# Kernel tuning notes

Measured on AMD Instinct MI355X. Metric: run time of the kernel, lower is better.

## Reference

```python
import jax, jax.numpy as jnp
import numpy as np

NEG = -1e30  # finite stand-in for log(0); safe for logaddexp and its gradient


def setup_inputs() -> dict:
    key = jax.random.key(0)
    k1, k2 = jax.random.split(key)
    B, T, C, U = 256, 512, 128, 128
    logits = jax.random.normal(k1, (B, T, C), dtype=jnp.float32)
    y_pred = jax.nn.softmax(logits, axis=-1)  # ctc_batch_cost expects probabilities
    y_true = jax.random.randint(k2, (B, U), 0, C - 1)  # labels exclude blank=C-1
    return {"y_true": y_true, "y_pred": y_pred}


def _ctc_batch_cost(y_true, y_pred):
    """Keras-style CTC: blank = num_classes-1, logp = log(y_pred + 1e-7),
    full input_length = T and label_length = U for every row (as in the layer).
    Returns loss of shape [B, 1]."""
    B, T, C = y_pred.shape
    U = y_true.shape[1]
    blank = C - 1
    S = 2 * U + 1  # extended label: blank-interleaved
    logp = jnp.log(y_pred + 1e-7)  # [B,T,C], keras epsilon

    # extended label sequence z = [blank, l1, blank, l2, ..., lU, blank]
    ext = jnp.full((B, S), blank, dtype=y_true.dtype).at[:, 1::2].set(y_true)

    # lp[t,b,s] = logp[b,t,ext[b,s]]
    lp = jnp.take_along_axis(logp, jnp.broadcast_to(ext[:, None, :], (B, T, S)), axis=2)
    lp = jnp.transpose(lp, (1, 0, 2))  # [T,B,S]

    # skip transition s-2 -> s allowed iff z[s] != blank and z[s] != z[s-2]
    ext_m2 = jnp.pad(ext, ((0, 0), (2, 0)), constant_values=blank)[:, :S]
    skip = (ext != blank) & (ext != ext_m2)
    skip = skip.at[:, :2].set(False)  # no s-2 predecessor for s in {0,1}

    alpha0 = jnp.full((B, S), NEG, dtype=logp.dtype)
    alpha0 = alpha0.at[:, 0].set(lp[0, :, 0]).at[:, 1].set(lp[0, :, 1])

    def step(a, lp_t):
        a1 = jnp.pad(a, ((0, 0), (1, 0)), constant_values=NEG)[:, :S]
        a2 = jnp.pad(a, ((0, 0), (2, 0)), constant_values=NEG)[:, :S]
        a2 = jnp.where(skip, a2, NEG)
        a = jnp.logaddexp(jnp.logaddexp(a, a1), a2) + lp_t
        return a, None

    aT, _ = jax.lax.scan(step, alpha0, lp[1:])
    loss = -jnp.logaddexp(aT[:, S - 1], aT[:, S - 2])
    return loss[:, None]  # [B,1], matching ctc_batch_cost output shape


def reference(y_true, y_pred):
    # The layer returns y_pred and registers the loss via add_loss; the loss is
    # the actual computation of interest, so we return it.
    return _ctc_batch_cost(y_true, y_pred)
```

## Files before the change

kernel.cpp:

```cpp
#include <hip/hip_runtime.h>

#define EPSF 1e-7f

typedef unsigned int u32;
typedef _Float16 h2_t __attribute__((ext_vector_type(2)));

#define DPPF0(x, ctrl) \
    __int_as_float(__builtin_amdgcn_update_dpp(0, __float_as_int(x), ctrl, 0xF, 0xF, false))

__device__ __forceinline__ float f_rcp(float x) { return __builtin_amdgcn_rcpf(x); }
__device__ __forceinline__ float wave_shr1_f(float x) { return DPPF0(x, 0x138); }

__device__ __forceinline__ float wave_max64(float x) {
    x = fmaxf(x, DPPF0(x, 0x111));
    x = fmaxf(x, DPPF0(x, 0x112));
    x = fmaxf(x, DPPF0(x, 0x114));
    x = fmaxf(x, DPPF0(x, 0x118));
    x = fmaxf(x, DPPF0(x, 0x142));
    x = fmaxf(x, DPPF0(x, 0x143));
    return __int_as_float(__builtin_amdgcn_readlane(__float_as_int(x), 63));
}

__device__ __forceinline__ float wave_sum64(float x) {
    x += DPPF0(x, 0x111);
    x += DPPF0(x, 0x112);
    x += DPPF0(x, 0x114);
    x += DPPF0(x, 0x118);
    x += DPPF0(x, 0x142);
    x += DPPF0(x, 0x143);
    return __int_as_float(__builtin_amdgcn_readlane(__float_as_int(x), 63));
}

#define STEPQ(PW_, PBE_) do { \
    const h2_t h_ = __builtin_bit_cast(h2_t, PW_); \
    const float rpb_ = f_rcp(PBE_); \
    const float q1 = ((float)h_.x + EPSF) * rpb_; \
    const float q3 = ((float)h_.y + EPSF) * rpb_; \
    const float n3 = wave_shr1_f(u3); \
    const float t1 = fmaf(m1, n3, u0 + u1); \
    const float t3 = fmaf(m3, u1, u2 + u3); \
    u4 = u4 + u3; \
    u3 = t3 * q3; \
    u2 = u2 + u1; \
    u1 = t1 * q1; \
    u0 = u0 + n3; \
} while (0)

#define SNAP2(RM, LM) do { \
    float mm_ = fmaxf(fmaxf(u0, u1), fmaxf(u2, fmaxf(u3, u4))); \
    mm_ = wave_max64(mm_); \
    RM = f_rcp(mm_); \
    LM = __logf(mm_); \
} while (0)

#define APPLY2(RM, LM) do { \
    u0 *= RM; u1 *= RM; u2 *= RM; u3 *= RM; u4 *= RM; \
    O += LM; \
} while (0)

#define LDW(X, BASE) do { \
    X##k0 = pkl[(BASE) + 0][lane]; X##k1 = pkl[(BASE) + 1][lane]; \
    X##k2 = pkl[(BASE) + 2][lane]; X##k3 = pkl[(BASE) + 3][lane]; \
    X##k4 = pkl[(BASE) + 4][lane]; X##k5 = pkl[(BASE) + 5][lane]; \
    X##k6 = pkl[(BASE) + 6][lane]; X##k7 = pkl[(BASE) + 7][lane]; \
    X##b0 = pbl[(BASE) + 0]; X##b1 = pbl[(BASE) + 1]; \
    X##b2 = pbl[(BASE) + 2]; X##b3 = pbl[(BASE) + 3]; \
    X##b4 = pbl[(BASE) + 4]; X##b5 = pbl[(BASE) + 5]; \
    X##b6 = pbl[(BASE) + 6]; X##b7 = pbl[(BASE) + 7]; \
} while (0)

#define CONS8W(X) do { \
    STEPQ(X##k0, X##b0 + EPSF); STEPQ(X##k1, X##b1 + EPSF); APPLY2(rmA, lmA); \
    STEPQ(X##k2, X##b2 + EPSF); STEPQ(X##k3, X##b3 + EPSF); SNAP2(rmB, lmB); \
    STEPQ(X##k4, X##b4 + EPSF); STEPQ(X##k5, X##b5 + EPSF); APPLY2(rmB, lmB); \
    STEPQ(X##k6, X##b6 + EPSF); STEPQ(X##k7, X##b7 + EPSF); SNAP2(rmA, lmA); \
} while (0)

#define CONS0W(X) do { \
    STEPQ(X##k1, X##b1 + EPSF); STEPQ(X##k2, X##b2 + EPSF); APPLY2(rmA, lmA); \
    STEPQ(X##k3, X##b3 + EPSF); STEPQ(X##k4, X##b4 + EPSF); SNAP2(rmB, lmB); \
    STEPQ(X##k5, X##b5 + EPSF); STEPQ(X##k6, X##b6 + EPSF); APPLY2(rmB, lmB); \
    STEPQ(X##k7, X##b7 + EPSF); SNAP2(rmA, lmA); \
} while (0)

__global__ __launch_bounds__(256, 1) void ctc_fused512(
        const int* __restrict__ y_true, const float* __restrict__ y_pred,
        float* __restrict__ out) {
    __shared__ u32   pkl[512][64];
    __shared__ float pbl[512];

    const int b    = blockIdx.x;
    const int tid  = threadIdx.x;
    const int w    = tid >> 6;
    const int lane = tid & 63;
    const float* __restrict__ yp = y_pred + (size_t)b * (512 * 128);

    const int2 lc = ((const int2*)(y_true + (size_t)b * 128))[lane];
    const int c1 = lc.x, c3 = lc.y;

    {
        const int t0 = w * 128;
        const float* __restrict__ rp = yp + (size_t)t0 * 128;
#pragma unroll 8
        for (int r = 0; r < 128; ++r) {
            const float p1 = rp[r * 128 + c1];
            const float p3 = rp[r * 128 + c3];
            const u32 wd = (u32)__builtin_bit_cast(unsigned short, (_Float16)p1)
                         | ((u32)__builtin_bit_cast(unsigned short, (_Float16)p3) << 16);
            pkl[t0 + r][lane] = wd;
        }
        pbl[t0 + lane]      = rp[(size_t)lane * 128 + 127];
        pbl[t0 + 64 + lane] = rp[(size_t)(64 + lane) * 128 + 127];
    }
    __syncthreads();
    if (w != 0) return;

    const int cp = __builtin_amdgcn_update_dpp(0, c3, 0x138, 0xF, 0xF, false);
    const float m1 = (lane > 0 && c1 != cp) ? 1.f : 0.f;
    const float m3 = (c3 != c1) ? 1.f : 0.f;

    float bls = 0.f;
#pragma unroll
    for (int k = 0; k < 8; ++k) {
        const int t = lane * 8 + k;
        if (t >= 1) bls += __logf(pbl[t] + EPSF);
    }
    bls = wave_sum64(bls);

    float u0, u1, u2 = 0.f, u3 = 0.f, u4 = 0.f;
    u0 = (lane == 0) ? yp[127] + EPSF : 0.f;
    u1 = (lane == 0) ? yp[c1] + EPSF : 0.f;
    float O = 0.f;
    float rmA = 1.0f, lmA = 0.0f, rmB = 1.0f, lmB = 0.0f;

    u32 Ak0, Ak1, Ak2, Ak3, Ak4, Ak5, Ak6, Ak7;
    u32 Bk0, Bk1, Bk2, Bk3, Bk4, Bk5, Bk6, Bk7;
    float Ab0, Ab1, Ab2, Ab3, Ab4, Ab5, Ab6, Ab7;
    float Bb0, Bb1, Bb2, Bb3, Bb4, Bb5, Bb6, Bb7;

    LDW(A, 0);
    LDW(B, 8);
    CONS0W(A);

    for (int j = 0; j < 31; ++j) {
        LDW(A, 16 * j + 16); CONS8W(B);
        LDW(B, 16 * j + 24); CONS8W(A);
    }
    CONS8W(B);

    if (lane == 63) out[b] = -(O + bls + __logf(u3 + u4));
}

__global__ __launch_bounds__(64, 1) void ctc_scan_generic(
        const int* __restrict__ y_true, const float* __restrict__ y_pred,
        float* __restrict__ out, int T, int C, int U) {
    const int b    = blockIdx.x;
    const int lane = threadIdx.x;
    const int blank = C - 1;
    const float* __restrict__ yp = y_pred + (size_t)b * T * C;

    const int2 lc = ((const int2*)(y_true + (size_t)b * U))[lane];
    const int c1 = lc.x, c3 = lc.y;
    const int cp = __builtin_amdgcn_update_dpp(0, c3, 0x138, 0xF, 0xF, false);
    const float m1 = (lane > 0 && c1 != cp) ? 1.f : 0.f;
    const float m3 = (c3 != c1) ? 1.f : 0.f;

    float u0, u1, u2 = 0.f, u3 = 0.f, u4 = 0.f;
    u0 = (lane == 0) ? yp[blank] + EPSF : 0.f;
    u1 = (lane == 0) ? yp[c1] + EPSF : 0.f;
    float O = 0.f;
    float rmA = 1.0f, lmA = 0.0f;
    int kren = 0;

    for (int t = 1; t < T; ++t) {
        const float* row = yp + (size_t)t * C;
        const float pbe = row[blank] + EPSF;
        const float rpb = f_rcp(pbe);
        const float q1  = (row[c1] + EPSF) * rpb;
        const float q3  = (row[c3] + EPSF) * rpb;
        const float n3  = wave_shr1_f(u3);
        const float t1  = fmaf(m1, n3, u0 + u1);
        const float t3  = fmaf(m3, u1, u2 + u3);
        u4 = u4 + u3;
        u3 = t3 * q3;
        u2 = u2 + u1;
        u1 = t1 * q1;
        u0 = u0 + n3;
        O += __logf(pbe);
        if (++kren == 4) { SNAP2(rmA, lmA); APPLY2(rmA, lmA); kren = 0; }
    }
    if (lane == 63) out[b] = -(O + __logf(u3 + u4));
}

extern "C" void kernel_launch(void* const* d_in, const int* in_sizes, int n_in,
                              void* d_out, int out_size, void* d_ws, size_t ws_size,
                              hipStream_t stream) {
    const int*   y_true = (const int*)d_in[0];
    const float* y_pred = (const float*)d_in[1];
    float*       out    = (float*)d_out;

    const int B = out_size;
    const int U = in_sizes[0] / B;
    const int C = 128;
    const int T = in_sizes[1] / (B * C);

    if (T == 512 && C == 128 && U == 128) {
        ctc_fused512<<<B, 256, 0, stream>>>(y_true, y_pred, out);
    } else {
        ctc_scan_generic<<<B, 64, 0, stream>>>(y_true, y_pred, out, T, C, U);
    }
}
```

Measured before the change: 51.48 us.

## Stage y_pred rows through LDS with coalesced loads and precompute bf16 ratios

Replaces the per-lane gather of label probabilities from global memory with coalesced float4 loads of 32-row tiles into a shared staging buffer, double-buffered through registers. All four waves now compute the blank-normalised ratios q1,q3 during the prologue and pack them as bf16 pairs, so the serial scan wave no longer needs a reciprocal and extra per-step multiply. The aim is to cut uncoalesced global traffic and shorten the serial critical path. It adds 32 barriers and more shared memory, and bf16 ratios carry less mantissa precision than the previous fp16 probabilities.

```diff
diff --git a/kernel.cpp b/kernel.cpp
--- a/kernel.cpp
+++ b/kernel.cpp
@@ -3,7 +3,6 @@
 #define EPSF 1e-7f
 
 typedef unsigned int u32;
-typedef _Float16 h2_t __attribute__((ext_vector_type(2)));
 
 #define DPPF0(x, ctrl) \
     __int_as_float(__builtin_amdgcn_update_dpp(0, __float_as_int(x), ctrl, 0xF, 0xF, false))
@@ -31,11 +30,17 @@
     return __int_as_float(__builtin_amdgcn_readlane(__float_as_int(x), 63));
 }
 
-#define STEPQ(PW_, PBE_) do { \
-    const h2_t h_ = __builtin_bit_cast(h2_t, PW_); \
-    const float rpb_ = f_rcp(PBE_); \
-    const float q1 = ((float)h_.x + EPSF) * rpb_; \
-    const float q3 = ((float)h_.y + EPSF) * rpb_; \
+__device__ __forceinline__ u32 pack_bf2(float a, float b) {
+    u32 ua = __float_as_uint(a), ub = __float_as_uint(b);
+    ua += 0x7FFFu + ((ua >> 16) & 1u);
+    ub += 0x7FFFu + ((ub >> 16) & 1u);
+    return (ua >> 16) | (ub & 0xFFFF0000u);
+}
+
+#define STEPQ(PW_) do { \
+    const u32 w_ = (PW_); \
+    const float q1 = __uint_as_float(w_ << 16); \
+    const float q3 = __uint_as_float(w_ & 0xFFFF0000u); \
     const float n3 = wave_shr1_f(u3); \
     const float t1 = fmaf(m1, n3, u0 + u1); \
     const float t3 = fmaf(m3, u1, u2 + u3); \
@@ -59,35 +64,32 @@
 } while (0)
 
 #define LDW(X, BASE) do { \
-    X##k0 = pkl[(BASE) + 0][lane]; X##k1 = pkl[(BASE) + 1][lane]; \
-    X##k2 = pkl[(BASE) + 2][lane]; X##k3 = pkl[(BASE) + 3][lane]; \
-    X##k4 = pkl[(BASE) + 4][lane]; X##k5 = pkl[(BASE) + 5][lane]; \
-    X##k6 = pkl[(BASE) + 6][lane]; X##k7 = pkl[(BASE) + 7][lane]; \
-    X##b0 = pbl[(BASE) + 0]; X##b1 = pbl[(BASE) + 1]; \
-    X##b2 = pbl[(BASE) + 2]; X##b3 = pbl[(BASE) + 3]; \
-    X##b4 = pbl[(BASE) + 4]; X##b5 = pbl[(BASE) + 5]; \
-    X##b6 = pbl[(BASE) + 6]; X##b7 = pbl[(BASE) + 7]; \
+    X##0 = qkl[(BASE) + 0][lane]; X##1 = qkl[(BASE) + 1][lane]; \
+    X##2 = qkl[(BASE) + 2][lane]; X##3 = qkl[(BASE) + 3][lane]; \
+    X##4 = qkl[(BASE) + 4][lane]; X##5 = qkl[(BASE) + 5][lane]; \
+    X##6 = qkl[(BASE) + 6][lane]; X##7 = qkl[(BASE) + 7][lane]; \
 } while (0)
 
 #define CONS8W(X) do { \
-    STEPQ(X##k0, X##b0 + EPSF); STEPQ(X##k1, X##b1 + EPSF); APPLY2(rmA, lmA); \
-    STEPQ(X##k2, X##b2 + EPSF); STEPQ(X##k3, X##b3 + EPSF); SNAP2(rmB, lmB); \
-    STEPQ(X##k4, X##b4 + EPSF); STEPQ(X##k5, X##b5 + EPSF); APPLY2(rmB, lmB); \
-    STEPQ(X##k6, X##b6 + EPSF); STEPQ(X##k7, X##b7 + EPSF); SNAP2(rmA, lmA); \
+    STEPQ(X##0); STEPQ(X##1); APPLY2(rmA, lmA); \
+    STEPQ(X##2); STEPQ(X##3); SNAP2(rmB, lmB); \
+    STEPQ(X##4); STEPQ(X##5); APPLY2(rmB, lmB); \
+    STEPQ(X##6); STEPQ(X##7); SNAP2(rmA, lmA); \
 } while (0)
 
 #define CONS0W(X) do { \
-    STEPQ(X##k1, X##b1 + EPSF); STEPQ(X##k2, X##b2 + EPSF); APPLY2(rmA, lmA); \
-    STEPQ(X##k3, X##b3 + EPSF); STEPQ(X##k4, X##b4 + EPSF); SNAP2(rmB, lmB); \
-    STEPQ(X##k5, X##b5 + EPSF); STEPQ(X##k6, X##b6 + EPSF); APPLY2(rmB, lmB); \
-    STEPQ(X##k7, X##b7 + EPSF); SNAP2(rmA, lmA); \
-} while (0)
-
-__global__ __launch_bounds__(256, 1) void ctc_fused512(
+    STEPQ(X##1); STEPQ(X##2); APPLY2(rmA, lmA); \
+    STEPQ(X##3); STEPQ(X##4); SNAP2(rmB, lmB); \
+    STEPQ(X##5); STEPQ(X##6); APPLY2(rmB, lmB); \
+    STEPQ(X##7); SNAP2(rmA, lmA); \
+} while (0)
+
+__global__ __launch_bounds__(256, 1) void ctc_fused512b(
         const int* __restrict__ y_true, const float* __restrict__ y_pred,
         float* __restrict__ out) {
-    __shared__ u32   pkl[512][64];
+    __shared__ u32   qkl[512][64];
     __shared__ float pbl[512];
+    __shared__ float stage[32][128];
 
     const int b    = blockIdx.x;
     const int tid  = threadIdx.x;
@@ -98,21 +100,57 @@
     const int2 lc = ((const int2*)(y_true + (size_t)b * 128))[lane];
     const int c1 = lc.x, c3 = lc.y;
 
+    float4 rg[4];
     {
-        const int t0 = w * 128;
-        const float* __restrict__ rp = yp + (size_t)t0 * 128;
-#pragma unroll 8
-        for (int r = 0; r < 128; ++r) {
-            const float p1 = rp[r * 128 + c1];
-            const float p3 = rp[r * 128 + c3];
-            const u32 wd = (u32)__builtin_bit_cast(unsigned short, (_Float16)p1)
-                         | ((u32)__builtin_bit_cast(unsigned short, (_Float16)p3) << 16);
-            pkl[t0 + r][lane] = wd;
-        }
-        pbl[t0 + lane]      = rp[(size_t)lane * 128 + 127];
-        pbl[t0 + 64 + lane] = rp[(size_t)(64 + lane) * 128 + 127];
+        const float* src = yp;
+#pragma unroll
+        for (int i = 0; i < 4; ++i) {
+            const int f = tid + i * 256;
+            rg[i] = *(const float4*)(src + (size_t)(f >> 5) * 128 + ((f & 31) << 2));
+        }
+#pragma unroll
+        for (int i = 0; i < 4; ++i) {
+            const int f = tid + i * 256;
+            *(float4*)(&stage[f >> 5][(f & 31) << 2]) = rg[i];
+        }
     }
     __syncthreads();
+
+    for (int k = 0; k < 16; ++k) {
+        if (k < 15) {
+            const float* src = yp + (size_t)(k + 1) * 32 * 128;
+#pragma unroll
+            for (int i = 0; i < 4; ++i) {
+                const int f = tid + i * 256;
+                rg[i] = *(const float4*)(src + (size_t)(f >> 5) * 128 + ((f & 31) << 2));
+            }
+        }
+        {
+            const int cb = k * 32;
+#pragma unroll
+            for (int rr = 0; rr < 8; ++rr) {
+                const int r = w * 8 + rr;
+                const float pv1 = stage[r][c1];
+                const float pv3 = stage[r][c3];
+                const float pvb = stage[r][127];
+                const float rpb = f_rcp(pvb + EPSF);
+                const float q1  = (pv1 + EPSF) * rpb;
+                const float q3  = (pv3 + EPSF) * rpb;
+                qkl[cb + r][lane] = pack_bf2(q1, q3);
+            }
+            if (tid < 32) pbl[cb + tid] = stage[tid][127];
+        }
+        __syncthreads();
+        if (k < 15) {
+#pragma unroll
+            for (int i = 0; i < 4; ++i) {
+                const int f = tid + i * 256;
+                *(float4*)(&stage[f >> 5][(f & 31) << 2]) = rg[i];
+            }
+        }
+        __syncthreads();
+    }
+
     if (w != 0) return;
 
     const int cp = __builtin_amdgcn_update_dpp(0, c3, 0x138, 0xF, 0xF, false);
@@ -121,8 +159,8 @@
 
     float bls = 0.f;
 #pragma unroll
-    for (int k = 0; k < 8; ++k) {
-        const int t = lane * 8 + k;
+    for (int kk = 0; kk < 8; ++kk) {
+        const int t = lane * 8 + kk;
         if (t >= 1) bls += __logf(pbl[t] + EPSF);
     }
     bls = wave_sum64(bls);
@@ -133,10 +171,8 @@
     float O = 0.f;
     float rmA = 1.0f, lmA = 0.0f, rmB = 1.0f, lmB = 0.0f;
 
-    u32 Ak0, Ak1, Ak2, Ak3, Ak4, Ak5, Ak6, Ak7;
-    u32 Bk0, Bk1, Bk2, Bk3, Bk4, Bk5, Bk6, Bk7;
-    float Ab0, Ab1, Ab2, Ab3, Ab4, Ab5, Ab6, Ab7;
-    float Bb0, Bb1, Bb2, Bb3, Bb4, Bb5, Bb6, Bb7;
+    u32 A0, A1, A2, A3, A4, A5, A6, A7;
+    u32 B0, B1, B2, B3, B4, B5, B6, B7;
 
     LDW(A, 0);
     LDW(B, 8);
@@ -205,7 +241,7 @@
     const int T = in_sizes[1] / (B * C);
 
     if (T == 512 && C == 128 && U == 128) {
-        ctc_fused512<<<B, 256, 0, stream>>>(y_true, y_pred, out);
+        ctc_fused512b<<<B, 256, 0, stream>>>(y_true, y_pred, out);
     } else {
         ctc_scan_generic<<<B, 64, 0, stream>>>(y_true, y_pred, out, T, C, U);
     }
```

Result: slower. 53.17 us (+3.3%).

## Stream CTC probabilities through a 4-slot LDS ring with producer/consumer waves

Applied to the files above, without the earlier changes.

Replaces the load-everything-then-scan structure with a producer/consumer pipeline. Three producer waves gather label and blank probabilities chunk by chunk into a 4-slot shared ring, precompute the ratio q=(p+eps)/(pblank+eps) and the blank log-sum, and pack the ratios as bf16. The single scan wave spins on per-slot flags and consumes chunks as they arrive, so global loads overlap the serial recurrence and the reciprocal and logs move off the critical path. This adds spin-wait synchronisation overhead and uses bf16 instead of fp16, which lowers the precision of the ratios.

```diff
diff --git a/kernel.cpp b/kernel.cpp
--- a/kernel.cpp
+++ b/kernel.cpp
@@ -3,7 +3,6 @@
 #define EPSF 1e-7f
 
 typedef unsigned int u32;
-typedef _Float16 h2_t __attribute__((ext_vector_type(2)));
 
 #define DPPF0(x, ctrl) \
     __int_as_float(__builtin_amdgcn_update_dpp(0, __float_as_int(x), ctrl, 0xF, 0xF, false))
@@ -21,21 +20,17 @@
     return __int_as_float(__builtin_amdgcn_readlane(__float_as_int(x), 63));
 }
 
-__device__ __forceinline__ float wave_sum64(float x) {
-    x += DPPF0(x, 0x111);
-    x += DPPF0(x, 0x112);
-    x += DPPF0(x, 0x114);
-    x += DPPF0(x, 0x118);
-    x += DPPF0(x, 0x142);
-    x += DPPF0(x, 0x143);
-    return __int_as_float(__builtin_amdgcn_readlane(__float_as_int(x), 63));
-}
-
-#define STEPQ(PW_, PBE_) do { \
-    const h2_t h_ = __builtin_bit_cast(h2_t, PW_); \
-    const float rpb_ = f_rcp(PBE_); \
-    const float q1 = ((float)h_.x + EPSF) * rpb_; \
-    const float q3 = ((float)h_.y + EPSF) * rpb_; \
+__device__ __forceinline__ u32 pack_bf2(float a, float b) {
+    u32 ua = __float_as_uint(a), ub = __float_as_uint(b);
+    ua += 0x7FFFu + ((ua >> 16) & 1u);
+    ub += 0x7FFFu + ((ub >> 16) & 1u);
+    return (ua >> 16) | (ub & 0xFFFF0000u);
+}
+
+#define STEPQ(W_) do { \
+    const u32 w_ = (W_); \
+    const float q1 = __uint_as_float(w_ << 16); \
+    const float q3 = __uint_as_float(w_ & 0xFFFF0000u); \
     const float n3 = wave_shr1_f(u3); \
     const float t1 = fmaf(m1, n3, u0 + u1); \
     const float t3 = fmaf(m3, u1, u2 + u3); \
@@ -58,36 +53,27 @@
     O += LM; \
 } while (0)
 
-#define LDW(X, BASE) do { \
-    X##k0 = pkl[(BASE) + 0][lane]; X##k1 = pkl[(BASE) + 1][lane]; \
-    X##k2 = pkl[(BASE) + 2][lane]; X##k3 = pkl[(BASE) + 3][lane]; \
-    X##k4 = pkl[(BASE) + 4][lane]; X##k5 = pkl[(BASE) + 5][lane]; \
-    X##k6 = pkl[(BASE) + 6][lane]; X##k7 = pkl[(BASE) + 7][lane]; \
-    X##b0 = pbl[(BASE) + 0]; X##b1 = pbl[(BASE) + 1]; \
-    X##b2 = pbl[(BASE) + 2]; X##b3 = pbl[(BASE) + 3]; \
-    X##b4 = pbl[(BASE) + 4]; X##b5 = pbl[(BASE) + 5]; \
-    X##b6 = pbl[(BASE) + 6]; X##b7 = pbl[(BASE) + 7]; \
-} while (0)
-
-#define CONS8W(X) do { \
-    STEPQ(X##k0, X##b0 + EPSF); STEPQ(X##k1, X##b1 + EPSF); APPLY2(rmA, lmA); \
-    STEPQ(X##k2, X##b2 + EPSF); STEPQ(X##k3, X##b3 + EPSF); SNAP2(rmB, lmB); \
-    STEPQ(X##k4, X##b4 + EPSF); STEPQ(X##k5, X##b5 + EPSF); APPLY2(rmB, lmB); \
-    STEPQ(X##k6, X##b6 + EPSF); STEPQ(X##k7, X##b7 + EPSF); SNAP2(rmA, lmA); \
-} while (0)
-
-#define CONS0W(X) do { \
-    STEPQ(X##k1, X##b1 + EPSF); STEPQ(X##k2, X##b2 + EPSF); APPLY2(rmA, lmA); \
-    STEPQ(X##k3, X##b3 + EPSF); STEPQ(X##k4, X##b4 + EPSF); SNAP2(rmB, lmB); \
-    STEPQ(X##k5, X##b5 + EPSF); STEPQ(X##k6, X##b6 + EPSF); APPLY2(rmB, lmB); \
-    STEPQ(X##k7, X##b7 + EPSF); SNAP2(rmA, lmA); \
-} while (0)
-
-__global__ __launch_bounds__(256, 1) void ctc_fused512(
+#define CONS8Q(I0) do { \
+    STEPQ(q[(I0)+0]); STEPQ(q[(I0)+1]); APPLY2(rm1, lm1); \
+    STEPQ(q[(I0)+2]); STEPQ(q[(I0)+3]); SNAP2(rm2, lm2); \
+    STEPQ(q[(I0)+4]); STEPQ(q[(I0)+5]); APPLY2(rm2, lm2); \
+    STEPQ(q[(I0)+6]); STEPQ(q[(I0)+7]); SNAP2(rm1, lm1); \
+} while (0)
+
+#define CONS0Q() do { \
+    STEPQ(q[1]); STEPQ(q[2]); APPLY2(rm1, lm1); \
+    STEPQ(q[3]); STEPQ(q[4]); SNAP2(rm2, lm2); \
+    STEPQ(q[5]); STEPQ(q[6]); APPLY2(rm2, lm2); \
+    STEPQ(q[7]); SNAP2(rm1, lm1); \
+} while (0)
+
+__global__ __launch_bounds__(256, 1) void ctc_ring512(
         const int* __restrict__ y_true, const float* __restrict__ y_pred,
         float* __restrict__ out) {
-    __shared__ u32   pkl[512][64];
-    __shared__ float pbl[512];
+    __shared__ u32   qbuf[4][64][33];
+    __shared__ int   flags[4];
+    __shared__ int   cons_prog;
+    __shared__ float blsw[4];
 
     const int b    = blockIdx.x;
     const int tid  = threadIdx.x;
@@ -98,56 +84,71 @@
     const int2 lc = ((const int2*)(y_true + (size_t)b * 128))[lane];
     const int c1 = lc.x, c3 = lc.y;
 
-    {
-        const int t0 = w * 128;
-        const float* __restrict__ rp = yp + (size_t)t0 * 128;
-#pragma unroll 8
-        for (int r = 0; r < 128; ++r) {
-            const float p1 = rp[r * 128 + c1];
-            const float p3 = rp[r * 128 + c3];
-            const u32 wd = (u32)__builtin_bit_cast(unsigned short, (_Float16)p1)
-                         | ((u32)__builtin_bit_cast(unsigned short, (_Float16)p3) << 16);
-            pkl[t0 + r][lane] = wd;
+    if (tid < 4) flags[tid] = 0;
+    if (tid == 4) cons_prog = 0;
+    __syncthreads();
+
+    if (w != 0) {
+        float bls = 0.f;
+        for (int c = 0; c < 16; ++c) {
+            if (c >= 4) {
+                while (__hip_atomic_load(&cons_prog, __ATOMIC_ACQUIRE,
+                                         __HIP_MEMORY_SCOPE_WORKGROUP) < c - 3)
+                    __builtin_amdgcn_s_sleep(2);
+            }
+            const int s = c & 3;
+#pragma unroll
+            for (int k = 0; k < 11; ++k) {
+                const int j = (w - 1) + 3 * k;
+                if (j < 32) {
+                    const int t = c * 32 + j;
+                    const float* rowp = yp + (size_t)t * 128;
+                    const float p1  = rowp[c1];
+                    const float p3  = rowp[c3];
+                    const float pbe = rowp[127] + EPSF;
+                    const float rpb = f_rcp(pbe);
+                    qbuf[s][lane][j] = pack_bf2((p1 + EPSF) * rpb,
+                                                (p3 + EPSF) * rpb);
+                    if (t >= 1) bls += __logf(pbe);
+                }
+            }
+            if (c == 15 && lane == 0) blsw[w] = bls;
+            if (lane == 0)
+                __hip_atomic_fetch_add(&flags[s], 1, __ATOMIC_RELEASE,
+                                       __HIP_MEMORY_SCOPE_WORKGROUP);
         }
-        pbl[t0 + lane]      = rp[(size_t)lane * 128 + 127];
-        pbl[t0 + 64 + lane] = rp[(size_t)(64 + lane) * 128 + 127];
-    }
-    __syncthreads();
-    if (w != 0) return;
+        return;
+    }
 
     const int cp = __builtin_amdgcn_update_dpp(0, c3, 0x138, 0xF, 0xF, false);
     const float m1 = (lane > 0 && c1 != cp) ? 1.f : 0.f;
     const float m3 = (c3 != c1) ? 1.f : 0.f;
 
-    float bls = 0.f;
+    float u0 = (lane == 0) ? yp[127] + EPSF : 0.f;
+    float u1 = (lane == 0) ? yp[c1] + EPSF : 0.f;
+    float u2 = 0.f, u3 = 0.f, u4 = 0.f;
+    float O = 0.f;
+    float rm1 = 1.f, lm1 = 0.f, rm2 = 1.f, lm2 = 0.f;
+
+    for (int c = 0; c < 16; ++c) {
+        const int s = c & 3;
+        const int need = 3 * ((c >> 2) + 1);
+        while (__hip_atomic_load(&flags[s], __ATOMIC_ACQUIRE,
+                                 __HIP_MEMORY_SCOPE_WORKGROUP) < need)
+            ;
+        u32 q[32];
 #pragma unroll
-    for (int k = 0; k < 8; ++k) {
-        const int t = lane * 8 + k;
-        if (t >= 1) bls += __logf(pbl[t] + EPSF);
-    }
-    bls = wave_sum64(bls);
-
-    float u0, u1, u2 = 0.f, u3 = 0.f, u4 = 0.f;
-    u0 = (lane == 0) ? yp[127] + EPSF : 0.f;
-    u1 = (lane == 0) ? yp[c1] + EPSF : 0.f;
-    float O = 0.f;
-    float rmA = 1.0f, lmA = 0.0f, rmB = 1.0f, lmB = 0.0f;
-
-    u32 Ak0, Ak1, Ak2, Ak3, Ak4, Ak5, Ak6, Ak7;
-    u32 Bk0, Bk1, Bk2, Bk3, Bk4, Bk5, Bk6, Bk7;
-    float Ab0, Ab1, Ab2, Ab3, Ab4, Ab5, Ab6, Ab7;
-    float Bb0, Bb1, Bb2, Bb3, Bb4, Bb5, Bb6, Bb7;
-
-    LDW(A, 0);
-    LDW(B, 8);
-    CONS0W(A);
-
-    for (int j = 0; j < 31; ++j) {
-        LDW(A, 16 * j + 16); CONS8W(B);
-        LDW(B, 16 * j + 24); CONS8W(A);
-    }
-    CONS8W(B);
-
+        for (int i = 0; i < 32; ++i) q[i] = qbuf[s][lane][i];
+        if (c == 0) { CONS0Q(); } else { CONS8Q(0); }
+        CONS8Q(8);
+        CONS8Q(16);
+        CONS8Q(24);
+        if (lane == 0)
+            __hip_atomic_store(&cons_prog, c + 1, __ATOMIC_RELEASE,
+                               __HIP_MEMORY_SCOPE_WORKGROUP);
+    }
+
+    const float bls = blsw[1] + blsw[2] + blsw[3];
     if (lane == 63) out[b] = -(O + bls + __logf(u3 + u4));
 }
 
@@ -165,11 +166,11 @@
     const float m1 = (lane > 0 && c1 != cp) ? 1.f : 0.f;
     const float m3 = (c3 != c1) ? 1.f : 0.f;
 
-    float u0, u1, u2 = 0.f, u3 = 0.f, u4 = 0.f;
-    u0 = (lane == 0) ? yp[blank] + EPSF : 0.f;
-    u1 = (lane == 0) ? yp[c1] + EPSF : 0.f;
+    float u0 = (lane == 0) ? yp[blank] + EPSF : 0.f;
+    float u1 = (lane == 0) ? yp[c1] + EPSF : 0.f;
+    float u2 = 0.f, u3 = 0.f, u4 = 0.f;
     float O = 0.f;
-    float rmA = 1.0f, lmA = 0.0f;
+    float rm1 = 1.0f, lm1 = 0.0f;
     int kren = 0;
 
     for (int t = 1; t < T; ++t) {
@@ -187,7 +188,15 @@
         u1 = t1 * q1;
         u0 = u0 + n3;
         O += __logf(pbe);
-        if (++kren == 4) { SNAP2(rmA, lmA); APPLY2(rmA, lmA); kren = 0; }
+        if (++kren == 4) {
+            float mm_ = fmaxf(fmaxf(u0, u1), fmaxf(u2, fmaxf(u3, u4)));
+            mm_ = wave_max64(mm_);
+            rm1 = f_rcp(mm_);
+            lm1 = __logf(mm_);
+            u0 *= rm1; u1 *= rm1; u2 *= rm1; u3 *= rm1; u4 *= rm1;
+            O += lm1;
+            kren = 0;
+        }
     }
     if (lane == 63) out[b] = -(O + __logf(u3 + u4));
 }
@@ -205,7 +214,7 @@
     const int T = in_sizes[1] / (B * C);
 
     if (T == 512 && C == 128 && U == 128) {
-        ctc_fused512<<<B, 256, 0, stream>>>(y_true, y_pred, out);
+        ctc_ring512<<<B, 256, 0, stream>>>(y_true, y_pred, out);
     } else {
         ctc_scan_generic<<<B, 64, 0, stream>>>(y_true, y_pred, out, T, C, U);
     }
```

New measurement: 53.85 us. 1.05x slower.
